# Kernel tuning notes

Hardware: AMD Instinct MI355X
Metric: run time of the kernel (lower is better)

## Reference

```python
import jax, jax.numpy as jnp
import numpy as np

B, N, D, E, H = 16, 1024, 1024, 4, 16


def setup_inputs() -> dict:
    key = jax.random.key(0)
    k1, k2, k3, k4 = jax.random.split(key, 4)
    return {
        "input_tokens": jax.random.normal(k1, (B, N, D), dtype=jnp.float32),
        "expert_mask": jax.random.randint(k2, (B, N), 0, E, dtype=jnp.int32),
        "qkv_w": jax.random.normal(k3, (3 * D, D), dtype=jnp.float32) * 0.02,
        "proj_w": jax.random.normal(k4, (D, D), dtype=jnp.float32) * 0.02,
        "proj_b": jnp.zeros((D,), dtype=jnp.float32),
    }


def reference(input_tokens, expert_mask, qkv_w, proj_w, proj_b):
    b, n, d = input_tokens.shape
    hd = d // H
    scale = 1.0 / np.sqrt(hd).astype(np.float32)
    # nested expert e uses first d_e = D / 2^(E-1-e) features (expert E-1 = full dim)
    d_tok = d // (2 ** (E - 1 - expert_mask))                     # [B, N]
    feat_mask = (jnp.arange(d)[None, None, :] < d_tok[..., None]).astype(input_tokens.dtype)  # [B, N, D]
    # NestedLinearExpand: slice input features per token (== mask), full 3D output
    x_in = input_tokens * feat_mask
    qkv = jnp.einsum('bnd,fd->bnf', x_in, qkv_w).reshape(b, n, 3, H, hd)
    q, k, v = jnp.moveaxis(qkv, 2, 0)                             # each [B, N, H, hd]
    q = q.transpose(0, 2, 1, 3)                                   # [B, H, N, hd]
    k = k.transpose(0, 2, 1, 3)
    v = v.transpose(0, 2, 1, 3)
    scores = jnp.einsum('bhqd,bhkd->bhqk', q, k) * scale          # [B, H, N, N]
    attn = jax.nn.softmax(scores, axis=-1)
    x = jnp.einsum('bhqk,bhkd->bhqd', attn, v)                    # [B, H, N, hd]
    x = x.transpose(0, 2, 1, 3).reshape(b, n, d)
    # NestedLinearContract: full-dim matmul, only first d_e outputs kept per token
    y = jnp.einsum('bnd,fd->bnf', x, proj_w) + proj_b
    return y * feat_mask
```

## Files before the change

### kernel.cpp

```cpp
#include <hip/hip_runtime.h>
#include <hip/hip_bf16.h>


typedef __bf16 bf16_t;
typedef __bf16 bf16x8 __attribute__((ext_vector_type(8)));
typedef __bf16 bf16x4 __attribute__((ext_vector_type(4)));
typedef float f32x4 __attribute__((ext_vector_type(4)));
typedef float f32x16 __attribute__((ext_vector_type(16)));
typedef int i32x4 __attribute__((ext_vector_type(4)));

typedef __attribute__((address_space(1))) void gvoid;
typedef __attribute__((address_space(3))) void lvoid;

#define MFMA16(a, b, c) __builtin_amdgcn_mfma_f32_16x16x32_bf16((a), (b), (c), 0, 0, 0)
#define MFMA32(a, b, c) __builtin_amdgcn_mfma_f32_32x32x16_bf16((a), (b), (c), 0, 0, 0)
#define GLOAD_LDS16(gsrc, ldst) \
  __builtin_amdgcn_global_load_lds((gvoid*)(gsrc), (lvoid*)(ldst), 16, 0, 0)

#define QSCALE 0.18033688f

__device__ __forceinline__ unsigned cvtpk(float lo, float hi) {
  unsigned r;
  asm("v_cvt_pk_bf16_f32 %0, %1, %2" : "=v"(r) : "v"(lo), "v"(hi));
  return r;
}
__device__ __forceinline__ void pl32swap(unsigned& x, unsigned& y) {
  asm("v_permlane32_swap_b32 %0, %1" : "+v"(x), "+v"(y));
}

__global__ __launch_bounds__(256) void prep_tokens(
    const float* __restrict__ x, const int* __restrict__ em,
    bf16_t* __restrict__ xq) {
  const int row = blockIdx.x;
  const int dt = 128 << em[row];
  const int d = threadIdx.x * 4;
  float4 v = ((const float4*)(x + (size_t)row * 1024))[threadIdx.x];
  const bool keep = d < dt;
  bf16x4 o;
  o[0] = (bf16_t)(keep ? v.x : 0.f);
  o[1] = (bf16_t)(keep ? v.y : 0.f);
  o[2] = (bf16_t)(keep ? v.z : 0.f);
  o[3] = (bf16_t)(keep ? v.w : 0.f);
  *((bf16x4*)(xq + (size_t)row * 1024 + d)) = o;
}

__global__ __launch_bounds__(256) void conv_w(
    const float* __restrict__ s, bf16_t* __restrict__ dvec) {
  const int i = blockIdx.x * 256 + threadIdx.x;
  float4 v = ((const float4*)s)[i];
  bf16x4 o;
  o[0] = (bf16_t)v.x; o[1] = (bf16_t)v.y; o[2] = (bf16_t)v.z; o[3] = (bf16_t)v.w;
  ((bf16x4*)dvec)[i] = o;
}

template <int EPI, int NCOL>
__global__ __launch_bounds__(512, 2) void gemm256(
    const bf16_t* __restrict__ A, const bf16_t* __restrict__ Bw, int K,
    bf16_t* __restrict__ qo, bf16_t* __restrict__ ko, bf16_t* __restrict__ vto,
    float* __restrict__ yout, const float* __restrict__ bias,
    const int* __restrict__ em) {
  __shared__ bf16_t lds[2][32768];
  const int tid = threadIdx.x;
  const int lane = tid & 63, w = tid >> 6;
  const int wm = w >> 2, wn = w & 3;
  const int g = lane >> 4, c16 = lane & 15;

  const int nwg = gridDim.x;
  const int lb = ((int)blockIdx.x & 7) * (nwg >> 3) + ((int)blockIdx.x >> 3);
  const int rowbase = (lb / NCOL) * 256;
  const int colbase = (lb % NCOL) * 256;

  const int trow = tid >> 3;
  const int scol = (((tid & 7) ^ (trow & 7)) << 3);
  const bf16_t* pa = A + (size_t)(rowbase + trow) * K + scol;
  const bf16_t* pb = Bw + (size_t)(colbase + trow) * K + scol;

#define STAGE(j, koff, dst)                                       \
  GLOAD_LDS16(((j) < 4 ? pa + (size_t)((j) * 64) * K              \
                       : pb + (size_t)(((j) - 4) * 64) * K) +     \
                  (koff),                                         \
              (dst) + ((j) * 512 + tid) * 8)

#define LDFRAG(base, R, kk)            \
  (*(const bf16x8*)((base) + (size_t)(R) * 64 + \
                    (((((kk) << 2) + g) ^ (c16 & 7)) << 3)))

  f32x4 acc[8][4] = {};

#pragma unroll
  for (int j = 0; j < 8; ++j) STAGE(j, 0, (bf16_t*)lds[0]);
  asm volatile("s_waitcnt vmcnt(0)" ::: "memory");
  __builtin_amdgcn_s_barrier();

  const int NT = K >> 6;
  for (int t = 0; t < NT; ++t) {
    const bf16_t* Lb = lds[t & 1];
    const bf16_t* LbB = Lb + 16384;
    const bool pf = (t + 1) < NT;

    if (pf) {
      bf16_t* Sd = (bf16_t*)lds[(t + 1) & 1];
      const int koff = (t + 1) << 6;
#pragma unroll
      for (int j = 0; j < 8; ++j) STAGE(j, koff, Sd);
    }

    bf16x8 af[4][2], af2[4][2], b0[2][2], b1[2][2];
#pragma unroll
    for (int mi = 0; mi < 4; ++mi)
#pragma unroll
      for (int kk = 0; kk < 2; ++kk)
        af[mi][kk] = LDFRAG(Lb, wm * 128 + mi * 16 + c16, kk);
#pragma unroll
    for (int ni = 0; ni < 2; ++ni)
#pragma unroll
      for (int kk = 0; kk < 2; ++kk)
        b0[ni][kk] = LDFRAG(LbB, wn * 64 + ni * 16 + c16, kk);
#pragma unroll
    for (int mi = 0; mi < 4; ++mi)
#pragma unroll
      for (int ni = 0; ni < 2; ++ni)
#pragma unroll
        for (int kk = 0; kk < 2; ++kk)
          acc[mi][ni] = MFMA16(af[mi][kk], b0[ni][kk], acc[mi][ni]);

#pragma unroll
    for (int ni = 0; ni < 2; ++ni)
#pragma unroll
      for (int kk = 0; kk < 2; ++kk)
        b1[ni][kk] = LDFRAG(LbB, wn * 64 + (ni + 2) * 16 + c16, kk);
#pragma unroll
    for (int mi = 0; mi < 4; ++mi)
#pragma unroll
      for (int ni = 0; ni < 2; ++ni)
#pragma unroll
        for (int kk = 0; kk < 2; ++kk)
          acc[mi][ni + 2] = MFMA16(af[mi][kk], b1[ni][kk], acc[mi][ni + 2]);

#pragma unroll
    for (int mi = 0; mi < 4; ++mi)
#pragma unroll
      for (int kk = 0; kk < 2; ++kk)
        af2[mi][kk] = LDFRAG(Lb, wm * 128 + (mi + 4) * 16 + c16, kk);
#pragma unroll
    for (int mi = 0; mi < 4; ++mi)
#pragma unroll
      for (int ni = 0; ni < 2; ++ni)
#pragma unroll
        for (int kk = 0; kk < 2; ++kk)
          acc[mi + 4][ni] = MFMA16(af2[mi][kk], b0[ni][kk], acc[mi + 4][ni]);

#pragma unroll
    for (int mi = 0; mi < 4; ++mi)
#pragma unroll
      for (int ni = 0; ni < 2; ++ni)
#pragma unroll
        for (int kk = 0; kk < 2; ++kk)
          acc[mi + 4][ni + 2] = MFMA16(af2[mi][kk], b1[ni][kk], acc[mi + 4][ni + 2]);

    if (pf) asm volatile("s_waitcnt vmcnt(0)" ::: "memory");
    __builtin_amdgcn_s_barrier();
  }

  if constexpr (EPI == 0) {
    const int s = colbase >> 10;
#pragma unroll
    for (int mi = 0; mi < 8; ++mi)
#pragma unroll
      for (int ni = 0; ni < 4; ++ni)
#pragma unroll
        for (int j = 0; j < 4; ++j) {
          const int row = rowbase + wm * 128 + mi * 16 + g * 4 + j;
          const int col = colbase + wn * 64 + ni * 16 + c16;
          const float v = acc[mi][ni][j];
          const int bb = row >> 10, n = row & 1023;
          const int h = (col >> 6) & 15, e = col & 63;
          const size_t bh = (size_t)(bb * 16 + h);
          if (s == 0)
            qo[(bh * 1024 + n) * 64 + e] = (bf16_t)(v * QSCALE);
          else if (s == 1)
            ko[(bh * 1024 + n) * 64 + e] = (bf16_t)v;
          else
            vto[(bh * 64 + e) * 1024 + n] = (bf16_t)v;
        }
  } else {
#pragma unroll
    for (int mi = 0; mi < 8; ++mi)
#pragma unroll
      for (int j = 0; j < 4; ++j) {
        const int row = rowbase + wm * 128 + mi * 16 + g * 4 + j;
        const int dt = 128 << em[row];
#pragma unroll
        for (int ni = 0; ni < 4; ++ni) {
          const int col = colbase + wn * 64 + ni * 16 + c16;
          const float v = acc[mi][ni][j] + bias[col];
          yout[(size_t)row * 1024 + col] = (col < dt) ? v : 0.f;
        }
      }
  }
#undef STAGE
#undef LDFRAG
}

__global__ __launch_bounds__(512, 2) void attn256(
    const bf16_t* __restrict__ Q, const bf16_t* __restrict__ Kb,
    const bf16_t* __restrict__ VT, bf16_t* __restrict__ X) {
  __shared__ bf16_t Klds[2][4096];
  __shared__ bf16_t Vlds[2][4096];
  const int tid = threadIdx.x;
  const int w = tid >> 6, lane = tid & 63;
  const int k32 = lane & 31, q5 = lane >> 5;
  const int bh = blockIdx.y;
  const int qbase = blockIdx.x * 256 + w * 32;

  const bf16_t* Qbh = Q + (size_t)bh * 65536;
  const bf16_t* Kbh = Kb + (size_t)bh * 65536;
  const bf16_t* Vbh = VT + (size_t)bh * 65536;

  const int trow = tid >> 3;
  const int tslot = (tid & 7) ^ (trow & 7);
  const bf16_t* kg = Kbh + (size_t)trow * 64 + tslot * 8;
  const bf16_t* vg = Vbh + (size_t)trow * 1024 + tslot * 8;

  bf16x8 qf[4];
#pragma unroll
  for (int kc = 0; kc < 4; ++kc)
    qf[kc] = *(const bf16x8*)(Qbh + (size_t)(qbase + k32) * 64 + kc * 16 + q5 * 8);
  asm volatile("" ::"v"(qf[0]), "v"(qf[1]), "v"(qf[2]), "v"(qf[3]));

  const int rbase = k32 * 128 + q5 * 16;
  const int rswz = (k32 & 7) << 4;

  f32x16 O0 = {}, O1 = {};
  float m = -3.0e38f, lsum = 0.f;

  GLOAD_LDS16(kg, (bf16_t*)Klds[0] + tid * 8);
  GLOAD_LDS16(vg, (bf16_t*)Vlds[0] + tid * 8);

  for (int step = 0; step < 16; ++step) {
    const int buf = step & 1;
    if (step < 15) {
      GLOAD_LDS16(kg + (step + 1) * 4096, (bf16_t*)Klds[buf ^ 1] + tid * 8);
      GLOAD_LDS16(vg + (step + 1) * 64, (bf16_t*)Vlds[buf ^ 1] + tid * 8);
      asm volatile("s_waitcnt vmcnt(2)" ::: "memory");
    } else {
      asm volatile("s_waitcnt vmcnt(0)" ::: "memory");
    }
    __builtin_amdgcn_s_barrier();

    const char* Kl = (const char*)Klds[buf];
    const char* Vl = (const char*)Vlds[buf];

    f32x16 S0 = {}, S1 = {};
#pragma unroll
    for (int kc = 0; kc < 4; ++kc) {
      const int off = (rbase + kc * 32) ^ rswz;
      bf16x8 kf0 = *(const bf16x8*)(Kl + off);
      bf16x8 kf1 = *(const bf16x8*)(Kl + off + 4096);
      S0 = MFMA32(kf0, qf[kc], S0);
      S1 = MFMA32(kf1, qf[kc], S1);
    }

    float pm = fmaxf(S0[0], S1[0]);
#pragma unroll
    for (int r = 1; r < 16; ++r) pm = fmaxf(pm, fmaxf(S0[r], S1[r]));
    pm = fmaxf(pm, __shfl_xor(pm, 32));
    if (__any(pm > m + 8.f)) {
      const float mnew = fmaxf(m, pm);
      const float corr = __builtin_amdgcn_exp2f(m - mnew);
      m = mnew;
      lsum *= corr;
      const int ci = __builtin_bit_cast(int, corr);
#pragma unroll
      for (int r = 0; r < 16; ++r) {
        const int qsel = (r & 3) + 8 * (r >> 2) + 4 * q5;
        const float cr = __builtin_bit_cast(
            float, __builtin_amdgcn_ds_bpermute(qsel << 2, ci));
        O0[r] *= cr;
        O1[r] *= cr;
      }
    }
    float ps = 0.f;
#pragma unroll
    for (int r = 0; r < 16; ++r) {
      float p = __builtin_amdgcn_exp2f(S0[r] - m);
      ps += p; S0[r] = p;
      p = __builtin_amdgcn_exp2f(S1[r] - m);
      ps += p; S1[r] = p;
    }
    lsum += ps;

#define MAKE_PA(PV, B0, PA)                            \
  {                                                    \
    unsigned a_ = cvtpk(PV[B0 + 0], PV[B0 + 1]);       \
    unsigned b_ = cvtpk(PV[B0 + 2], PV[B0 + 3]);       \
    unsigned c_ = cvtpk(PV[B0 + 4], PV[B0 + 5]);       \
    unsigned d_ = cvtpk(PV[B0 + 6], PV[B0 + 7]);       \
    pl32swap(a_, c_);                                  \
    pl32swap(b_, d_);                                  \
    i32x4 wv_;                                         \
    wv_[0] = a_; wv_[1] = b_; wv_[2] = c_; wv_[3] = d_; \
    PA = __builtin_bit_cast(bf16x8, wv_);              \
  }
#define PV_STEP(PV, B0, KS)                                       \
  {                                                               \
    bf16x8 pa;                                                    \
    MAKE_PA(PV, B0, pa);                                          \
    const int voff = (rbase + (KS) * 32) ^ rswz;                  \
    bf16x8 vf0 = *(const bf16x8*)(Vl + voff);                     \
    bf16x8 vf1 = *(const bf16x8*)(Vl + voff + 4096);              \
    O0 = MFMA32(pa, vf0, O0);                                     \
    O1 = MFMA32(pa, vf1, O1);                                     \
  }
    PV_STEP(S0, 0, 0)
    PV_STEP(S0, 8, 1)
    PV_STEP(S1, 0, 2)
    PV_STEP(S1, 8, 3)

    __builtin_amdgcn_s_barrier();
  }

  lsum += __shfl_xor(lsum, 32);
  const float rinv = 1.f / lsum;
  const int ri = __builtin_bit_cast(int, rinv);
  const int bb = bh >> 4, h = bh & 15;
  bf16_t* Xb = X + (size_t)bb * 1024 * 1024 + h * 64;
#pragma unroll
  for (int r = 0; r < 16; ++r) {
    const int qsel = (r & 3) + 8 * (r >> 2) + 4 * q5;
    const float rv = __builtin_bit_cast(
        float, __builtin_amdgcn_ds_bpermute(qsel << 2, ri));
    const size_t rowoff = (size_t)(qbase + qsel) * 1024;
    Xb[rowoff + k32] = (bf16_t)(O0[r] * rv);
    Xb[rowoff + 32 + k32] = (bf16_t)(O1[r] * rv);
  }
}

extern "C" void kernel_launch(void* const* d_in, const int* in_sizes, int n_in,
                              void* d_out, int out_size, void* d_ws,
                              size_t ws_size, hipStream_t stream) {
  const float* x = (const float*)d_in[0];
  const int* em = (const int*)d_in[1];
  const float* qkvw = (const float*)d_in[2];
  const float* projw = (const float*)d_in[3];
  const float* projb = (const float*)d_in[4];
  float* out = (float*)d_out;

  char* ws = (char*)d_ws;
  size_t off = 0;
  bf16_t* xin = (bf16_t*)(ws + off); off += (size_t)16384 * 1024 * 2;
  bf16_t* wq  = (bf16_t*)(ws + off); off += (size_t)3072 * 1024 * 2;
  bf16_t* wp  = (bf16_t*)(ws + off); off += (size_t)1024 * 1024 * 2;
  bf16_t* Qb  = (bf16_t*)(ws + off); off += (size_t)256 * 1024 * 64 * 2;
  bf16_t* Kb  = (bf16_t*)(ws + off); off += (size_t)256 * 1024 * 64 * 2;
  bf16_t* VTb = (bf16_t*)(ws + off); off += (size_t)256 * 64 * 1024 * 2;

  prep_tokens<<<16384, 256, 0, stream>>>(x, em, xin);
  conv_w<<<3072, 256, 0, stream>>>(qkvw, wq);
  conv_w<<<1024, 256, 0, stream>>>(projw, wp);

  gemm256<0, 12><<<768, 512, 0, stream>>>(
      xin, wq, 1024, Qb, Kb, VTb, nullptr, nullptr, nullptr);

  attn256<<<dim3(4, 256), 512, 0, stream>>>(Qb, Kb, VTb, xin);

  gemm256<1, 4><<<256, 512, 0, stream>>>(
      xin, wp, 1024, nullptr, nullptr, nullptr, out, projb, em);
}
```

Measured before the change: 320.3 us.

## Sort tokens by expert to skip masked K and output tiles in GEMMs

Adds a histogram, scan and scatter pass that builds a permutation grouping tokens by nested-expert index. Both GEMMs gather their A rows through this permutation. The QKV GEMM shortens its K loop to the largest active feature width in each 256-row tile. The projection GEMM writes zeros directly for column tiles lying entirely beyond every token's width instead of computing them. This removes the multiply work on features that are known to be zero. The cost is four small extra launches, gathered row loads, and the loss of the earlier workgroup swizzle for cache locality.

```diff
diff --git a/kernel.cpp b/kernel.cpp
--- a/kernel.cpp
+++ b/kernel.cpp
@@ -26,6 +26,43 @@
 }
 __device__ __forceinline__ void pl32swap(unsigned& x, unsigned& y) {
   asm("v_permlane32_swap_b32 %0, %1" : "+v"(x), "+v"(y));
+}
+
+__global__ void zero_s(int* s) { if (threadIdx.x < 12) s[threadIdx.x] = 0; }
+
+__global__ __launch_bounds__(256) void hist_experts(
+    const int* __restrict__ em, int* __restrict__ s) {
+  const int t = blockIdx.x * 256 + threadIdx.x;
+  const int e = em[t];
+  const int lane = threadIdx.x & 63;
+#pragma unroll
+  for (int x = 0; x < 4; ++x) {
+    const unsigned long long mk = __ballot(e == x);
+    if (mk && lane == (int)__ffsll((unsigned long long)mk) - 1)
+      atomicAdd(&s[x], (int)__popcll(mk));
+  }
+}
+
+__global__ void scan_s(int* s) {
+  s[4] = 0; s[5] = s[0]; s[6] = s[0] + s[1]; s[7] = s[0] + s[1] + s[2];
+}
+
+__global__ __launch_bounds__(256) void scatter_experts(
+    const int* __restrict__ em, int* __restrict__ s, int* __restrict__ perm) {
+  const int t = blockIdx.x * 256 + threadIdx.x;
+  const int e = em[t];
+  const int lane = threadIdx.x & 63;
+  const unsigned long long below = ((unsigned long long)1 << lane) - 1;
+#pragma unroll
+  for (int x = 0; x < 4; ++x) {
+    const unsigned long long mk = __ballot(e == x);
+    if (mk == 0) continue;
+    const int leader = (int)__ffsll((unsigned long long)mk) - 1;
+    int b = 0;
+    if (lane == leader) b = atomicAdd(&s[8 + x], (int)__popcll(mk));
+    b = __shfl(b, leader);
+    if (e == x) perm[s[4 + x] + b + (int)__popcll(mk & below)] = t;
+  }
 }
 
 __global__ __launch_bounds__(256) void prep_tokens(
@@ -53,9 +90,10 @@
   ((bf16x4*)dvec)[i] = o;
 }
 
-template <int EPI, int NCOL>
+template <int EPI>
 __global__ __launch_bounds__(512, 2) void gemm256(
     const bf16_t* __restrict__ A, const bf16_t* __restrict__ Bw, int K,
+    const int* __restrict__ perm,
     bf16_t* __restrict__ qo, bf16_t* __restrict__ ko, bf16_t* __restrict__ vto,
     float* __restrict__ yout, const float* __restrict__ bias,
     const int* __restrict__ em) {
@@ -65,20 +103,39 @@
   const int wm = w >> 2, wn = w & 3;
   const int g = lane >> 4, c16 = lane & 15;
 
-  const int nwg = gridDim.x;
-  const int lb = ((int)blockIdx.x & 7) * (nwg >> 3) + ((int)blockIdx.x >> 3);
-  const int rowbase = (lb / NCOL) * 256;
-  const int colbase = (lb % NCOL) * 256;
+  const int bid = blockIdx.x;
+  const int rowbase = (bid & 63) * 256;
+  const int colbase = (bid >> 6) * 256;
+
+  const int dtmax = 128 << em[perm[rowbase + 255]];
+
+  if constexpr (EPI == 1) {
+    if (colbase >= dtmax) {
+      const float4 z = make_float4(0.f, 0.f, 0.f, 0.f);
+#pragma unroll
+      for (int i = 0; i < 32; ++i) {
+        const int idx = i * 512 + tid;
+        const int r = idx >> 6, c4 = idx & 63;
+        const int ro = perm[rowbase + r];
+        ((float4*)(yout + (size_t)ro * 1024 + colbase))[c4] = z;
+      }
+      return;
+    }
+  }
+
+  const int NT = (EPI == 0) ? (dtmax >> 6) : (K >> 6);
 
   const int trow = tid >> 3;
   const int scol = (((tid & 7) ^ (trow & 7)) << 3);
-  const bf16_t* pa = A + (size_t)(rowbase + trow) * K + scol;
-  const bf16_t* pb = Bw + (size_t)(colbase + trow) * K + scol;
-
-#define STAGE(j, koff, dst)                                       \
-  GLOAD_LDS16(((j) < 4 ? pa + (size_t)((j) * 64) * K              \
-                       : pb + (size_t)(((j) - 4) * 64) * K) +     \
-                  (koff),                                         \
+  const bf16_t* pA[4];
+#pragma unroll
+  for (int j = 0; j < 4; ++j)
+    pA[j] = A + (size_t)perm[rowbase + trow + j * 64] * K + scol;
+  const bf16_t* pB = Bw + (size_t)(colbase + trow) * K + scol;
+
+#define STAGE(j, koff, dst)                                        \
+  GLOAD_LDS16(((j) < 4 ? pA[j] : pB + (size_t)(((j) - 4) * 64) * K) + \
+                  (koff),                                          \
               (dst) + ((j) * 512 + tid) * 8)
 
 #define LDFRAG(base, R, kk)            \
@@ -92,7 +149,6 @@
   asm volatile("s_waitcnt vmcnt(0)" ::: "memory");
   __builtin_amdgcn_s_barrier();
 
-  const int NT = K >> 6;
   for (int t = 0; t < NT; ++t) {
     const bf16_t* Lb = lds[t & 1];
     const bf16_t* LbB = Lb + 16384;
@@ -167,13 +223,13 @@
 #pragma unroll
     for (int mi = 0; mi < 8; ++mi)
 #pragma unroll
-      for (int ni = 0; ni < 4; ++ni)
-#pragma unroll
-        for (int j = 0; j < 4; ++j) {
-          const int row = rowbase + wm * 128 + mi * 16 + g * 4 + j;
+      for (int j = 0; j < 4; ++j) {
+        const int row = perm[rowbase + wm * 128 + mi * 16 + g * 4 + j];
+        const int bb = row >> 10, n = row & 1023;
+#pragma unroll
+        for (int ni = 0; ni < 4; ++ni) {
           const int col = colbase + wn * 64 + ni * 16 + c16;
           const float v = acc[mi][ni][j];
-          const int bb = row >> 10, n = row & 1023;
           const int h = (col >> 6) & 15, e = col & 63;
           const size_t bh = (size_t)(bb * 16 + h);
           if (s == 0)
@@ -183,12 +239,13 @@
           else
             vto[(bh * 64 + e) * 1024 + n] = (bf16_t)v;
         }
+      }
   } else {
 #pragma unroll
     for (int mi = 0; mi < 8; ++mi)
 #pragma unroll
       for (int j = 0; j < 4; ++j) {
-        const int row = rowbase + wm * 128 + mi * 16 + g * 4 + j;
+        const int row = perm[rowbase + wm * 128 + mi * 16 + g * 4 + j];
         const int dt = 128 << em[row];
 #pragma unroll
         for (int ni = 0; ni < 4; ++ni) {
@@ -354,16 +411,23 @@
   bf16_t* Qb  = (bf16_t*)(ws + off); off += (size_t)256 * 1024 * 64 * 2;
   bf16_t* Kb  = (bf16_t*)(ws + off); off += (size_t)256 * 1024 * 64 * 2;
   bf16_t* VTb = (bf16_t*)(ws + off); off += (size_t)256 * 64 * 1024 * 2;
+  int* scr    = (int*)(ws + off); off += 64;
+  int* perm   = (int*)(ws + off); off += 16384 * 4;
+
+  zero_s<<<1, 16, 0, stream>>>(scr);
+  hist_experts<<<64, 256, 0, stream>>>(em, scr);
+  scan_s<<<1, 1, 0, stream>>>(scr);
+  scatter_experts<<<64, 256, 0, stream>>>(em, scr, perm);
 
   prep_tokens<<<16384, 256, 0, stream>>>(x, em, xin);
   conv_w<<<3072, 256, 0, stream>>>(qkvw, wq);
   conv_w<<<1024, 256, 0, stream>>>(projw, wp);
 
-  gemm256<0, 12><<<768, 512, 0, stream>>>(
-      xin, wq, 1024, Qb, Kb, VTb, nullptr, nullptr, nullptr);
+  gemm256<0><<<768, 512, 0, stream>>>(
+      xin, wq, 1024, perm, Qb, Kb, VTb, nullptr, nullptr, em);
 
   attn256<<<dim3(4, 256), 512, 0, stream>>>(Qb, Kb, VTb, xin);
 
-  gemm256<1, 4><<<256, 512, 0, stream>>>(
-      xin, wp, 1024, nullptr, nullptr, nullptr, out, projb, em);
-}
+  gemm256<1><<<256, 512, 0, stream>>>(
+      xin, wp, 1024, perm, nullptr, nullptr, nullptr, out, projb, em);
+}
```

New measurement: 329.0 us. +2.7%, slower.

## Sort tokens by expert width to skip zero K-tiles and output tiles

Applied to the files above, without the earlier changes.

Adds a per-batch counting sort that groups tokens by expert id and permutes the token rows before the QKV GEMM. Each 256-row tile then only loops over K up to the widest active feature dimension, so the zero-masked input columns are not multiplied. The projection GEMM writes zeros directly for column tiles beyond the tile's max width and scatters its outputs back through the permutation. Attention is permutation-invariant within a batch, so the results are unchanged. The cost is an extra small kernel, indirect row indexing, load imbalance across tiles, and a plain block-index tile order that replaces the previous swizzled mapping.

```diff
diff --git a/kernel.cpp b/kernel.cpp
--- a/kernel.cpp
+++ b/kernel.cpp
@@ -28,20 +28,48 @@
   asm("v_permlane32_swap_b32 %0, %1" : "+v"(x), "+v"(y));
 }
 
+__global__ __launch_bounds__(256) void sort_batch(
+    const int* __restrict__ em, int* __restrict__ perm, int* __restrict__ ems) {
+  __shared__ int cnt[4], base[4], cur[4];
+  const int b = blockIdx.x, t = threadIdx.x;
+  if (t < 4) cnt[t] = 0;
+  __syncthreads();
+  int e[4];
+#pragma unroll
+  for (int i = 0; i < 4; ++i) {
+    e[i] = em[b * 1024 + t * 4 + i];
+    atomicAdd(&cnt[e[i]], 1);
+  }
+  __syncthreads();
+  if (t == 0) {
+    base[0] = 0; base[1] = cnt[0];
+    base[2] = cnt[0] + cnt[1]; base[3] = cnt[0] + cnt[1] + cnt[2];
+    cur[0] = cur[1] = cur[2] = cur[3] = 0;
+  }
+  __syncthreads();
+#pragma unroll
+  for (int i = 0; i < 4; ++i) {
+    const int pos = base[e[i]] + atomicAdd(&cur[e[i]], 1);
+    perm[b * 1024 + pos] = t * 4 + i;
+    ems[b * 1024 + pos] = e[i];
+  }
+}
+
 __global__ __launch_bounds__(256) void prep_tokens(
-    const float* __restrict__ x, const int* __restrict__ em,
-    bf16_t* __restrict__ xq) {
-  const int row = blockIdx.x;
-  const int dt = 128 << em[row];
+    const float* __restrict__ x, const int* __restrict__ perm,
+    const int* __restrict__ ems, bf16_t* __restrict__ xq) {
+  const int prow = blockIdx.x;
+  const int orig = (prow & ~1023) + perm[prow];
+  const int dt = 128 << ems[prow];
   const int d = threadIdx.x * 4;
-  float4 v = ((const float4*)(x + (size_t)row * 1024))[threadIdx.x];
+  float4 v = ((const float4*)(x + (size_t)orig * 1024))[threadIdx.x];
   const bool keep = d < dt;
   bf16x4 o;
   o[0] = (bf16_t)(keep ? v.x : 0.f);
   o[1] = (bf16_t)(keep ? v.y : 0.f);
   o[2] = (bf16_t)(keep ? v.z : 0.f);
   o[3] = (bf16_t)(keep ? v.w : 0.f);
-  *((bf16x4*)(xq + (size_t)row * 1024 + d)) = o;
+  *((bf16x4*)(xq + (size_t)prow * 1024 + d)) = o;
 }
 
 __global__ __launch_bounds__(256) void conv_w(
@@ -53,22 +81,39 @@
   ((bf16x4*)dvec)[i] = o;
 }
 
-template <int EPI, int NCOL>
+template <int EPI>
 __global__ __launch_bounds__(512, 2) void gemm256(
     const bf16_t* __restrict__ A, const bf16_t* __restrict__ Bw, int K,
+    const int* __restrict__ perm, const int* __restrict__ ems,
     bf16_t* __restrict__ qo, bf16_t* __restrict__ ko, bf16_t* __restrict__ vto,
-    float* __restrict__ yout, const float* __restrict__ bias,
-    const int* __restrict__ em) {
+    float* __restrict__ yout, const float* __restrict__ bias) {
   __shared__ bf16_t lds[2][32768];
   const int tid = threadIdx.x;
   const int lane = tid & 63, w = tid >> 6;
   const int wm = w >> 2, wn = w & 3;
   const int g = lane >> 4, c16 = lane & 15;
 
-  const int nwg = gridDim.x;
-  const int lb = ((int)blockIdx.x & 7) * (nwg >> 3) + ((int)blockIdx.x >> 3);
-  const int rowbase = (lb / NCOL) * 256;
-  const int colbase = (lb % NCOL) * 256;
+  const int bid = blockIdx.x;
+  const int rowbase = (bid & 63) * 256;
+  const int colbase = (bid >> 6) * 256;
+
+  const int dtmax = 128 << ems[rowbase + 255];
+
+  if constexpr (EPI == 1) {
+    if (colbase >= dtmax) {
+      const float4 z = make_float4(0.f, 0.f, 0.f, 0.f);
+#pragma unroll
+      for (int i = 0; i < 32; ++i) {
+        const int idx = i * 512 + tid;
+        const int r = idx >> 6, c4 = idx & 63;
+        const int orow = ((rowbase + r) & ~1023) + perm[rowbase + r];
+        ((float4*)(yout + (size_t)orow * 1024 + colbase))[c4] = z;
+      }
+      return;
+    }
+  }
+
+  const int NT = (EPI == 0) ? (dtmax >> 6) : (K >> 6);
 
   const int trow = tid >> 3;
   const int scol = (((tid & 7) ^ (trow & 7)) << 3);
@@ -92,7 +137,6 @@
   asm volatile("s_waitcnt vmcnt(0)" ::: "memory");
   __builtin_amdgcn_s_barrier();
 
-  const int NT = K >> 6;
   for (int t = 0; t < NT; ++t) {
     const bf16_t* Lb = lds[t & 1];
     const bf16_t* LbB = Lb + 16384;
@@ -167,13 +211,13 @@
 #pragma unroll
     for (int mi = 0; mi < 8; ++mi)
 #pragma unroll
-      for (int ni = 0; ni < 4; ++ni)
-#pragma unroll
-        for (int j = 0; j < 4; ++j) {
-          const int row = rowbase + wm * 128 + mi * 16 + g * 4 + j;
+      for (int j = 0; j < 4; ++j) {
+        const int row = rowbase + wm * 128 + mi * 16 + g * 4 + j;
+        const int bb = row >> 10, n = row & 1023;
+#pragma unroll
+        for (int ni = 0; ni < 4; ++ni) {
           const int col = colbase + wn * 64 + ni * 16 + c16;
           const float v = acc[mi][ni][j];
-          const int bb = row >> 10, n = row & 1023;
           const int h = (col >> 6) & 15, e = col & 63;
           const size_t bh = (size_t)(bb * 16 + h);
           if (s == 0)
@@ -183,18 +227,20 @@
           else
             vto[(bh * 64 + e) * 1024 + n] = (bf16_t)v;
         }
+      }
   } else {
 #pragma unroll
     for (int mi = 0; mi < 8; ++mi)
 #pragma unroll
       for (int j = 0; j < 4; ++j) {
         const int row = rowbase + wm * 128 + mi * 16 + g * 4 + j;
-        const int dt = 128 << em[row];
+        const int dt = 128 << ems[row];
+        const int orow = (row & ~1023) + perm[row];
 #pragma unroll
         for (int ni = 0; ni < 4; ++ni) {
           const int col = colbase + wn * 64 + ni * 16 + c16;
           const float v = acc[mi][ni][j] + bias[col];
-          yout[(size_t)row * 1024 + col] = (col < dt) ? v : 0.f;
+          yout[(size_t)orow * 1024 + col] = (col < dt) ? v : 0.f;
         }
       }
   }
@@ -354,16 +400,20 @@
   bf16_t* Qb  = (bf16_t*)(ws + off); off += (size_t)256 * 1024 * 64 * 2;
   bf16_t* Kb  = (bf16_t*)(ws + off); off += (size_t)256 * 1024 * 64 * 2;
   bf16_t* VTb = (bf16_t*)(ws + off); off += (size_t)256 * 64 * 1024 * 2;
-
-  prep_tokens<<<16384, 256, 0, stream>>>(x, em, xin);
+  int* perm   = (int*)(ws + off); off += 16384 * 4;
+  int* ems    = (int*)(ws + off); off += 16384 * 4;
+
+  sort_batch<<<16, 256, 0, stream>>>(em, perm, ems);
+
+  prep_tokens<<<16384, 256, 0, stream>>>(x, perm, ems, xin);
   conv_w<<<3072, 256, 0, stream>>>(qkvw, wq);
   conv_w<<<1024, 256, 0, stream>>>(projw, wp);
 
-  gemm256<0, 12><<<768, 512, 0, stream>>>(
-      xin, wq, 1024, Qb, Kb, VTb, nullptr, nullptr, nullptr);
+  gemm256<0><<<768, 512, 0, stream>>>(
+      xin, wq, 1024, perm, ems, Qb, Kb, VTb, nullptr, nullptr);
 
   attn256<<<dim3(4, 256), 512, 0, stream>>>(Qb, Kb, VTb, xin);
 
-  gemm256<1, 4><<<256, 512, 0, stream>>>(
-      xin, wp, 1024, nullptr, nullptr, nullptr, out, projb, em);
-}
+  gemm256<1><<<256, 512, 0, stream>>>(
+      xin, wp, 1024, perm, ems, nullptr, nullptr, nullptr, out, projb);
+}
```

After: 295.0 us. 1.09x faster.
